# Kernel tuning notes

Measured on AMD Instinct MI355X. Metric: run time of the kernel, lower is better.

## Reference

```python
import jax, jax.numpy as jnp
import numpy as np

B, NSP, H, W = 8, 1024, 256, 256   # frames, superpixels/frame, label-map size
N = B * NSP                        # total superpixel nodes
MIX = 0.5                          # mixing_coeff
SIGMA = 0.05


def _interp_axis(x, out, axis):
    # 1-D bilinear interpolation along `axis`, align_corners=True
    n = x.shape[axis]
    pos = jnp.linspace(0.0, n - 1.0, out).astype(x.dtype)
    i0 = jnp.floor(pos).astype(jnp.int32)
    i1 = jnp.minimum(i0 + 1, n - 1)
    wt = pos - i0.astype(x.dtype)
    shp = [1] * x.ndim
    shp[axis] = out
    wt = wt.reshape(shp)
    return jnp.take(x, i0, axis=axis) * (1 - wt) + jnp.take(x, i1, axis=axis) * wt


def _upsample_ac(x, oh, ow):
    # nn.UpsamplingBilinear2d (align_corners=True)
    if x.shape[2] == oh and x.shape[3] == ow:
        return x
    return _interp_axis(_interp_axis(x, oh, 2), ow, 3)


def _sp_pool(feats, seg):
    # upsample [B,C,h,w] to label resolution, then average features per superpixel -> [N, C]
    C = feats.shape[1]
    up = _upsample_ac(feats, H, W)
    vals = up.transpose(0, 2, 3, 1).reshape(-1, C)          # [B*H*W, C]
    sums = jax.ops.segment_sum(vals, seg, num_segments=N)
    cnt = jax.ops.segment_sum(jnp.ones((seg.shape[0],), vals.dtype), seg, num_segments=N)
    return sums / jnp.maximum(cnt, 1.0)[:, None]


def _gcn(x, Wm, b, src, dst, ew):
    # GCNConv(normalize=False): out_i = sum_{j->i} ew * (x_j @ W) + b
    h = x @ Wm
    agg = jax.ops.segment_sum(h[src] * ew[:, None], dst, num_segments=x.shape[0])
    return agg + b


def _coord_map():
    # channel 0 varies along dim2 (w), channel 1 varies along dim3 (h), both in [0,1]
    c0 = jnp.broadcast_to((jnp.arange(H, dtype=jnp.float32) / (H - 1))[:, None], (H, W))
    c1 = jnp.broadcast_to((jnp.arange(W, dtype=jnp.float32) / (W - 1))[None, :], (H, W))
    return jnp.broadcast_to(jnp.stack([c0, c1], 0)[None], (B, 2, H, W))


def setup_inputs() -> dict:
    key = jax.random.key(0)
    ks = jax.random.split(key, 12)
    labels = jax.random.randint(ks[0], (B, 1, H, W), 0, NSP, dtype=jnp.int32)
    skip0 = jax.random.normal(ks[1], (B, 512, 32, 32), jnp.float32)
    skip1 = jax.random.normal(ks[2], (B, 256, 64, 64), jnp.float32)
    skip2 = jax.random.normal(ks[3], (B, 256, 128, 128), jnp.float32)
    E = 131072
    edges_nn = jax.random.randint(ks[4], (2, E), 0, N, dtype=jnp.int32)
    negs = jax.random.randint(ks[5], (E,), 0, N, dtype=jnp.int32)
    W0 = jax.random.normal(ks[6], (512, 256), jnp.float32) / np.float32(np.sqrt(512))
    W1 = jax.random.normal(ks[7], (256, 256), jnp.float32) / np.float32(np.sqrt(256))
    W2 = jax.random.normal(ks[8], (256, 256), jnp.float32) / np.float32(np.sqrt(256))
    lin_w = jax.random.normal(ks[9], (256, 1), jnp.float32) / np.float32(np.sqrt(256))
    z = jnp.zeros((256,), jnp.float32)
    return {"labels": labels, "skip0": skip0, "skip1": skip1, "skip2": skip2,
            "edges_nn": edges_nn, "negs": negs,
            "W0": W0, "b0": z, "W1": W1, "b1": z, "W2": W2, "b2": z, "lin_w": lin_w}


def reference(labels, skip0, skip1, skip2, edges_nn, negs, W0, b0, W1, b1, W2, b2, lin_w):
    # per-pixel global superpixel id (offset per frame)
    seg = (labels.reshape(B, -1) + NSP * jnp.arange(B, dtype=labels.dtype)[:, None]).reshape(-1)
    src, dst = edges_nn[0], edges_nn[1]

    # pooled normalized coordinates per superpixel -> gaussian edge weights
    pc = _sp_pool(_coord_map(), seg)                        # [N, 2]
    dr = pc[src] - pc[dst]
    dist = jnp.linalg.norm(dr, axis=1)
    edge_attr = jnp.exp(-dist ** 2 / SIGMA)

    x = _sp_pool(skip0, seg)                                # [N, 512]
    layers = [(W0, b0, None), (W1, b1, skip1), (W2, b2, skip2)]
    for i, (Wm, b, sk) in enumerate(layers):
        if i > 0:
            x = (1 - MIX) * x + MIX * _sp_pool(sk, seg)
        x = jax.nn.relu(_gcn(x, Wm, b, src, dst, edge_attr))

    s = x @ lin_w                                           # [N, 1]
    dap = jax.nn.sigmoid(s[src] - s[dst])
    dan = jax.nn.sigmoid(s[src] - s[negs])
    return dan, dap, edge_attr
```

## Files before the change

### kernel.cpp

```cpp
#include <hip/hip_runtime.h>
#include <hip/hip_bf16.h>
#include <cstdint>
#include <cstddef>

#define BB 8
#define NSPX 1024
#define NNODE 8192
#define EE 131072
#define NPIX 524288
#define CH 256

using bf16 = __hip_bfloat16;
typedef unsigned int uint;
typedef unsigned long long u64;

__device__ __forceinline__ float blo(uint u) { return __uint_as_float(u << 16); }
__device__ __forceinline__ float bhi(uint u) { return __uint_as_float(u & 0xffff0000u); }

__global__ __launch_bounds__(256) void zero_kernel(int4* p, int n4) {
  int i = blockIdx.x * 256 + threadIdx.x;
  int stride = gridDim.x * 256;
  int4 z = make_int4(0, 0, 0, 0);
  for (; i < n4; i += stride) p[i] = z;
}

__global__ __launch_bounds__(256) void seg_cnt_kernel(const int* __restrict__ labels,
                                                      int* __restrict__ segb,
                                                      u64* __restrict__ packed) {
  int p = blockIdx.x * 256 + threadIdx.x;
  if (p >= NPIX) return;
  int b = p >> 16;
  int h = (p >> 8) & 255;
  int w = p & 255;
  int seg = labels[p] + (b << 10);
  segb[p] = seg;
  u64 enc = (1ULL << 48) | ((u64)h << 24) | (u64)w;
  atomicAdd(&packed[seg], enc);
}

__global__ __launch_bounds__(256) void rcnt_kernel(const u64* __restrict__ packed,
                                                   int* __restrict__ cnt, float* __restrict__ rcnt,
                                                   float* __restrict__ pch, float* __restrict__ pcw) {
  int n = blockIdx.x * 256 + threadIdx.x;
  if (n >= NNODE) return;
  u64 v = packed[n];
  int c = (int)(v >> 48);
  int sh = (int)((v >> 24) & 0xFFFFFF);
  int sw = (int)(v & 0xFFFFFF);
  cnt[n] = c;
  float r = 1.0f / (float)(c > 1 ? c : 1);
  rcnt[n] = r;
  pch[n] = (float)sh * r * (1.0f / 255.0f);
  pcw[n] = (float)sw * r * (1.0f / 255.0f);
}

__global__ __launch_bounds__(1024) void scan_kernel(const int* __restrict__ cin, int* __restrict__ coff) {
  __shared__ int ps[1024];
  int t = threadIdx.x;
  int base = t * 8;
  int v[8];
  int sum = 0;
#pragma unroll
  for (int i = 0; i < 8; ++i) {
    int x = cin[base + i];
    v[i] = sum;
    sum += x;
  }
  ps[t] = sum;
  __syncthreads();
  for (int off = 1; off < 1024; off <<= 1) {
    int x = (t >= off) ? ps[t - off] : 0;
    __syncthreads();
    ps[t] += x;
    __syncthreads();
  }
  int prev = (t == 0) ? 0 : ps[t - 1];
#pragma unroll
  for (int i = 0; i < 8; ++i) coff[base + i] = prev + v[i];
  if (t == 1023) coff[8192] = ps[1023];
}

__global__ __launch_bounds__(256) void edge_cnt_kernel(const int* __restrict__ dst, int* __restrict__ cnt_e) {
  int e = blockIdx.x * 256 + threadIdx.x;
  if (e < EE) atomicAdd(&cnt_e[dst[e]], 1);
}

__global__ __launch_bounds__(256) void edge_attr_kernel(const int* __restrict__ src, const int* __restrict__ dst,
                                                        const float* __restrict__ pch, const float* __restrict__ pcw,
                                                        float* __restrict__ ew, float* __restrict__ outp) {
  int e = blockIdx.x * 256 + threadIdx.x;
  if (e >= EE) return;
  int s1 = src[e], d1 = dst[e];
  float dh = pch[s1] - pch[d1];
  float dw = pcw[s1] - pcw[d1];
  float ea = expf(-(dh * dh + dw * dw) * 20.0f);
  ew[e] = ea;
  outp[2 * EE + e] = ea;
}

__global__ __launch_bounds__(256) void edge_scatter_kernel(const int* __restrict__ dst,
                                                           const int* __restrict__ src,
                                                           const float* __restrict__ ew,
                                                           const int* __restrict__ eoff,
                                                           int* __restrict__ ecur,
                                                           int* __restrict__ srcs,
                                                           float* __restrict__ ews) {
  int e = blockIdx.x * 256 + threadIdx.x;
  if (e >= EE) return;
  int d = dst[e];
  int pos = eoff[d] + atomicAdd(&ecur[d], 1);
  srcs[pos] = src[e];
  ews[pos] = ew[e];
}

__global__ __launch_bounds__(256) void pixel_scatter_kernel(const int* __restrict__ segb,
                                                            const int* __restrict__ poff,
                                                            int* __restrict__ pcur,
                                                            int* __restrict__ psorted) {
  int p = blockIdx.x * 256 + threadIdx.x;
  if (p >= NPIX) return;
  int s = segb[p];
  int pos = poff[s] + atomicAdd(&pcur[s], 1);
  psorted[pos] = p;
}

__global__ __launch_bounds__(256) void gemm_kmaj_bf16(const float* __restrict__ A,
                                                      const float* __restrict__ W,
                                                      bf16* __restrict__ out) {
  __shared__ float As[64][36];
  int b = blockIdx.z;
  int m0 = blockIdx.x * 32;
  int n0 = blockIdx.y * 128;
  int t = threadIdx.x;
  int ct = t & 31;
  int rm = t >> 5;
  int l8 = t & 7, kr = t >> 3;
  const float* Ab = A + (size_t)b * 512 * 1024;
  float4 acc[4];
#pragma unroll
  for (int i = 0; i < 4; ++i) acc[i] = make_float4(0.f, 0.f, 0.f, 0.f);
  for (int k0 = 0; k0 < 512; k0 += 64) {
#pragma unroll
    for (int pass = 0; pass < 2; ++pass) {
      int k = kr + pass * 32;
      float4 v = *(const float4*)&Ab[(size_t)(k0 + k) * 1024 + m0 + l8 * 4];
      *(float4*)&As[k][l8 * 4] = v;
    }
    __syncthreads();
#pragma unroll 8
    for (int k = 0; k < 64; ++k) {
      float4 a = *(const float4*)&As[k][rm * 4];
      float4 wv = *(const float4*)&W[(size_t)(k0 + k) * 256 + n0 + ct * 4];
      acc[0].x += a.x * wv.x; acc[0].y += a.x * wv.y; acc[0].z += a.x * wv.z; acc[0].w += a.x * wv.w;
      acc[1].x += a.y * wv.x; acc[1].y += a.y * wv.y; acc[1].z += a.y * wv.z; acc[1].w += a.y * wv.w;
      acc[2].x += a.z * wv.x; acc[2].y += a.z * wv.y; acc[2].z += a.z * wv.z; acc[2].w += a.z * wv.w;
      acc[3].x += a.w * wv.x; acc[3].y += a.w * wv.y; acc[3].z += a.w * wv.z; acc[3].w += a.w * wv.w;
    }
    __syncthreads();
  }
#pragma unroll
  for (int i = 0; i < 4; ++i) {
    int m = m0 + rm * 4 + i;
    __hip_bfloat162 lo = __float22bfloat162_rn(make_float2(acc[i].x, acc[i].y));
    __hip_bfloat162 hi = __float22bfloat162_rn(make_float2(acc[i].z, acc[i].w));
    uint2 pk = make_uint2(*reinterpret_cast<uint*>(&lo), *reinterpret_cast<uint*>(&hi));
    *(uint2*)&out[((size_t)b * 1024 + m) * 256 + n0 + ct * 4] = pk;
  }
}

__global__ __launch_bounds__(256) void transpose64_bf16(const float* __restrict__ src, bf16* __restrict__ dst,
                                                        int C, int P) {
  __shared__ float tile[64][65];
  int b = blockIdx.z;
  int p0 = blockIdx.x * 64;
  int c0 = blockIdx.y * 64;
  int t = threadIdx.x;
  int l16 = t & 15, r16 = t >> 4;
#pragma unroll
  for (int pass = 0; pass < 4; ++pass) {
    int c = r16 + pass * 16;
    float4 v = *(const float4*)&src[((size_t)b * C + c0 + c) * P + p0 + l16 * 4];
    tile[c][l16 * 4 + 0] = v.x;
    tile[c][l16 * 4 + 1] = v.y;
    tile[c][l16 * 4 + 2] = v.z;
    tile[c][l16 * 4 + 3] = v.w;
  }
  __syncthreads();
  int l8 = t & 7, r32 = t >> 3;
#pragma unroll
  for (int pass = 0; pass < 2; ++pass) {
    int p = r32 + pass * 32;
    uint r[4];
#pragma unroll
    for (int q = 0; q < 4; ++q) {
      __hip_bfloat162 h2 = __float22bfloat162_rn(make_float2(tile[l8 * 8 + 2 * q][p], tile[l8 * 8 + 2 * q + 1][p]));
      r[q] = *reinterpret_cast<uint*>(&h2);
    }
    *(uint4*)&dst[((size_t)b * P + p0 + p) * C + c0 + l8 * 8] = make_uint4(r[0], r[1], r[2], r[3]);
  }
}

__device__ __forceinline__ void accum8(float wt, uint4 u, float* a) {
  a[0] += wt * blo(u.x); a[1] += wt * bhi(u.x);
  a[2] += wt * blo(u.y); a[3] += wt * bhi(u.y);
  a[4] += wt * blo(u.z); a[5] += wt * bhi(u.z);
  a[6] += wt * blo(u.w); a[7] += wt * bhi(u.w);
}

template <int HS, int LPP>
__global__ __launch_bounds__(256) void gather_scale(const bf16* __restrict__ F,
                                                    const int* __restrict__ poff,
                                                    const int* __restrict__ psorted,
                                                    const float* __restrict__ rc,
                                                    float* __restrict__ pout) {
  constexpr int S = 256 / LPP;
  constexpr int CHUNK = LPP * 8;
  int blk = blockIdx.x;
  int n = ((blk & 7) << 10) | (blk >> 3);
  int b = n >> 10;
  int c0 = blockIdx.y * CHUNK;
  int t = threadIdx.x;
  int l = t & (LPP - 1);
  int s = t / LPP;
  const bf16* fb = F + (size_t)b * (HS * HS) * 256 + c0 + l * 8;
  const float fh = (float)(HS - 1) / 255.0f;
  int j1 = poff[n + 1];
  float acc[8];
#pragma unroll
  for (int i = 0; i < 8; ++i) acc[i] = 0.f;
  for (int j = poff[n] + s; j < j1; j += S) {
    int p = psorted[j];
    int h = (p >> 8) & 255, w = p & 255;
    float ph = h * fh, pw = w * fh;
    int i0 = (int)ph, j0 = (int)pw;
    float th = ph - (float)i0, tw = pw - (float)j0;
    int i1 = min(i0 + 1, HS - 1), jj1 = min(j0 + 1, HS - 1);
    float w11 = th * tw, w10 = th - w11, w01 = tw - w11, w00 = 1.f - th - tw + w11;
    uint4 u00 = *(const uint4*)(fb + (i0 * HS + j0) * 256);
    uint4 u01 = *(const uint4*)(fb + (i0 * HS + jj1) * 256);
    uint4 u10 = *(const uint4*)(fb + (i1 * HS + j0) * 256);
    uint4 u11 = *(const uint4*)(fb + (i1 * HS + jj1) * 256);
    accum8(w00, u00, acc);
    accum8(w01, u01, acc);
    accum8(w10, u10, acc);
    accum8(w11, u11, acc);
  }
  __shared__ float4 red4[512];
  red4[t * 2 + 0] = make_float4(acc[0], acc[1], acc[2], acc[3]);
  red4[t * 2 + 1] = make_float4(acc[4], acc[5], acc[6], acc[7]);
  __syncthreads();
  if (t < LPP * 2) {
    float r = rc[n];
    int l2 = t >> 1, half = t & 1;
    float4 sum = make_float4(0.f, 0.f, 0.f, 0.f);
#pragma unroll
    for (int ss = 0; ss < S; ++ss) {
      float4 v = red4[(ss * LPP + l2) * 2 + half];
      sum.x += v.x; sum.y += v.y; sum.z += v.z; sum.w += v.w;
    }
    sum.x *= r; sum.y *= r; sum.z *= r; sum.w *= r;
    *(float4*)&pout[(size_t)n * 256 + c0 + t * 4] = sum;
  }
}

__global__ __launch_bounds__(256) void gemm_mix_n256(const float* __restrict__ X, const float* __restrict__ Pl,
                                                     const float* __restrict__ W, float* __restrict__ out) {
  const int t = threadIdx.x;
  const int r0 = blockIdx.x * 16;
  const int cw = (t & 63) * 4;
  const int rg = (t >> 6) * 4;
  __shared__ float Xl[16][68];
  float4 acc[4];
#pragma unroll
  for (int i = 0; i < 4; ++i) acc[i] = make_float4(0.f, 0.f, 0.f, 0.f);
  for (int k0 = 0; k0 < 256; k0 += 64) {
#pragma unroll
    for (int l = 0; l < 4; ++l) {
      int idx = t + 256 * l;
      int r = idx >> 6, k = idx & 63;
      size_t a = (size_t)(r0 + r) * 256 + k0 + k;
      Xl[r][k] = 0.5f * (X[a] + Pl[a]);
    }
    __syncthreads();
#pragma unroll
    for (int k4 = 0; k4 < 64; k4 += 4) {
      float4 a[4];
#pragma unroll
      for (int i = 0; i < 4; ++i) a[i] = *(const float4*)&Xl[rg + i][k4];
#pragma unroll
      for (int kk = 0; kk < 4; ++kk) {
        float4 w = *(const float4*)&W[(size_t)(k0 + k4 + kk) * 256 + cw];
#pragma unroll
        for (int i = 0; i < 4; ++i) {
          float av = ((const float*)&a[i])[kk];
          acc[i].x += av * w.x;
          acc[i].y += av * w.y;
          acc[i].z += av * w.z;
          acc[i].w += av * w.w;
        }
      }
    }
    __syncthreads();
  }
#pragma unroll
  for (int i = 0; i < 4; ++i)
    *(float4*)&out[(size_t)(r0 + rg + i) * 256 + cw] = acc[i];
}

__global__ __launch_bounds__(256) void agg_kernel(const float* __restrict__ h, const float* __restrict__ bias,
                                                  const int* __restrict__ eoff,
                                                  const int* __restrict__ srcs, const float* __restrict__ ews,
                                                  float* __restrict__ xout) {
  int n = blockIdx.x;
  int c = threadIdx.x;
  int e0 = eoff[n], e1 = eoff[n + 1];
  float acc = 0.f;
  for (int j = e0; j < e1; ++j) {
    acc += ews[j] * h[((size_t)srcs[j] << 8) + c];
  }
  float v = acc + bias[c];
  xout[((size_t)n << 8) + c] = v > 0.f ? v : 0.f;
}

__global__ __launch_bounds__(256) void score_kernel(const float* __restrict__ x, const float* __restrict__ lw,
                                                    float* __restrict__ s) {
  int t = threadIdx.x;
  int n = blockIdx.x * 4 + (t >> 6);
  int lane = t & 63;
  const float* row = x + ((size_t)n << 8);
  float v = row[lane] * lw[lane] + row[lane + 64] * lw[lane + 64] +
            row[lane + 128] * lw[lane + 128] + row[lane + 192] * lw[lane + 192];
#pragma unroll
  for (int off = 32; off > 0; off >>= 1) v += __shfl_down(v, off, 64);
  if (lane == 0) s[n] = v;
}

__global__ __launch_bounds__(256) void out_kernel(const float* __restrict__ s, const int* __restrict__ src,
                                                  const int* __restrict__ dst, const int* __restrict__ negs,
                                                  float* __restrict__ outp) {
  int e = blockIdx.x * 256 + threadIdx.x;
  if (e >= EE) return;
  float ss = s[src[e]];
  float a = ss - s[negs[e]];
  float b = ss - s[dst[e]];
  outp[e] = 1.0f / (1.0f + expf(-a));
  outp[EE + e] = 1.0f / (1.0f + expf(-b));
}

extern "C" void kernel_launch(void* const* d_in, const int* in_sizes, int n_in,
                              void* d_out, int out_size, void* d_ws, size_t ws_size,
                              hipStream_t stream) {
  const int*   labels = (const int*)d_in[0];
  const float* skip0  = (const float*)d_in[1];
  const float* skip1  = (const float*)d_in[2];
  const float* skip2  = (const float*)d_in[3];
  const int*   edges  = (const int*)d_in[4];
  const int*   negs   = (const int*)d_in[5];
  const float* W0     = (const float*)d_in[6];
  const float* b0     = (const float*)d_in[7];
  const float* W1     = (const float*)d_in[8];
  const float* b1     = (const float*)d_in[9];
  const float* W2     = (const float*)d_in[10];
  const float* b2     = (const float*)d_in[11];
  const float* lw     = (const float*)d_in[12];
  const int* esrc = edges;
  const int* edst = edges + EE;
  float* outp = (float*)d_out;

  size_t o = 0;
  char* base = (char*)d_ws;
  auto alloc = [&](size_t bytes) -> void* {
    void* p = base + o;
    o += (bytes + 255) & ~(size_t)255;
    return p;
  };
  u64* packed  = (u64*)alloc(NNODE * 8);
  int* cnt_e   = (int*)alloc(NNODE * 4);
  int* ecur    = (int*)alloc(NNODE * 4);
  int* pcur    = (int*)alloc(NNODE * 4);
  size_t zbytes = o;
  int*   cntp    = (int*)alloc(NNODE * 4);
  float* rcnt    = (float*)alloc(NNODE * 4);
  float* pch     = (float*)alloc(NNODE * 4);
  float* pcw     = (float*)alloc(NNODE * 4);
  int*   poff    = (int*)alloc((NNODE + 1) * 4);
  int*   eoff    = (int*)alloc((NNODE + 1) * 4);
  int*   srcs    = (int*)alloc(EE * 4);
  float* ews     = (float*)alloc(EE * 4);
  int*   psorted = (int*)alloc(NPIX * 4);
  float* ewb     = (float*)alloc(EE * 4);
  int*   segb    = (int*)alloc(NPIX * 4);
  float* bufA    = (float*)alloc((size_t)NNODE * CH * 4);
  float* bufB    = (float*)alloc((size_t)NNODE * CH * 4);
  float* bufC    = (float*)alloc((size_t)NNODE * CH * 4);
  float* p1buf   = (float*)alloc((size_t)NNODE * CH * 4);
  float* p2buf   = (float*)alloc((size_t)NNODE * CH * 4);
  bf16*  F0b     = (bf16*)alloc((size_t)BB * 1024 * CH * 2);
  bf16*  F1t     = (bf16*)alloc((size_t)BB * 4096 * CH * 2);
  bf16*  F2t     = (bf16*)alloc((size_t)BB * 16384 * CH * 2);
  float* sbuf    = (float*)alloc(NNODE * 4);
  (void)ws_size; (void)n_in; (void)in_sizes; (void)out_size;

  zero_kernel<<<64, 256, 0, stream>>>((int4*)d_ws, (int)(zbytes / 16));
  seg_cnt_kernel<<<NPIX / 256, 256, 0, stream>>>(labels, segb, packed);
  rcnt_kernel<<<NNODE / 256, 256, 0, stream>>>(packed, cntp, rcnt, pch, pcw);
  scan_kernel<<<1, 1024, 0, stream>>>(cntp, poff);
  pixel_scatter_kernel<<<NPIX / 256, 256, 0, stream>>>(segb, poff, pcur, psorted);
  edge_cnt_kernel<<<EE / 256, 256, 0, stream>>>(edst, cnt_e);
  scan_kernel<<<1, 1024, 0, stream>>>(cnt_e, eoff);
  edge_attr_kernel<<<EE / 256, 256, 0, stream>>>(esrc, edst, pch, pcw, ewb, outp);
  edge_scatter_kernel<<<EE / 256, 256, 0, stream>>>(edst, esrc, ewb, eoff, ecur, srcs, ews);
  gemm_kmaj_bf16<<<dim3(32, 2, BB), 256, 0, stream>>>(skip0, W0, F0b);
  transpose64_bf16<<<dim3(4096 / 64, 4, BB), 256, 0, stream>>>(skip1, F1t, 256, 4096);
  transpose64_bf16<<<dim3(16384 / 64, 4, BB), 256, 0, stream>>>(skip2, F2t, 256, 16384);
  gather_scale<32, 32><<<dim3(NNODE, 1), 256, 0, stream>>>(F0b, poff, psorted, rcnt, bufA);
  gather_scale<64, 32><<<dim3(NNODE, 1), 256, 0, stream>>>(F1t, poff, psorted, rcnt, p1buf);
  gather_scale<128, 16><<<dim3(NNODE, 2), 256, 0, stream>>>(F2t, poff, psorted, rcnt, p2buf);
  agg_kernel<<<NNODE, 256, 0, stream>>>(bufA, b0, eoff, srcs, ews, bufB);
  gemm_mix_n256<<<NNODE / 16, 256, 0, stream>>>(bufB, p1buf, W1, bufC);
  agg_kernel<<<NNODE, 256, 0, stream>>>(bufC, b1, eoff, srcs, ews, bufA);
  gemm_mix_n256<<<NNODE / 16, 256, 0, stream>>>(bufA, p2buf, W2, bufC);
  agg_kernel<<<NNODE, 256, 0, stream>>>(bufC, b2, eoff, srcs, ews, bufB);
  score_kernel<<<NNODE / 4, 256, 0, stream>>>(bufB, lw, sbuf);
  out_kernel<<<EE / 256, 256, 0, stream>>>(sbuf, esrc, edst, negs, outp);
}
```

Baseline: 774.7 us.

## Fuse preprocessing kernels, merge skip0/skip1 gathers, store GCN features as bf16

Merges the pixel and edge counting, both prefix scans, and the pixel/edge scatter plus edge-attribute computation into combined launches, cutting the preprocessing launch count. The skip0 and skip1 gathers now share one pass over each superpixel's sorted pixel list. Edge source and weight are packed into one uint2 array. The GCN hidden features fed to aggregation are stored in bf16, with two channels per thread, to halve gather traffic. This trades some precision in the aggregated features for fewer launches and less memory traffic.

```diff
diff --git a/kernel.cpp b/kernel.cpp
--- a/kernel.cpp
+++ b/kernel.cpp
@@ -16,6 +16,10 @@
 
 __device__ __forceinline__ float blo(uint u) { return __uint_as_float(u << 16); }
 __device__ __forceinline__ float bhi(uint u) { return __uint_as_float(u & 0xffff0000u); }
+__device__ __forceinline__ uint packbf2(float a, float b) {
+  __hip_bfloat162 h = __float22bfloat162_rn(make_float2(a, b));
+  return *reinterpret_cast<uint*>(&h);
+}
 
 __global__ __launch_bounds__(256) void zero_kernel(int4* p, int n4) {
   int i = blockIdx.x * 256 + threadIdx.x;
@@ -24,22 +28,60 @@
   for (; i < n4; i += stride) p[i] = z;
 }
 
-__global__ __launch_bounds__(256) void seg_cnt_kernel(const int* __restrict__ labels,
-                                                      int* __restrict__ segb,
-                                                      u64* __restrict__ packed) {
-  int p = blockIdx.x * 256 + threadIdx.x;
-  if (p >= NPIX) return;
-  int b = p >> 16;
-  int h = (p >> 8) & 255;
-  int w = p & 255;
-  int seg = labels[p] + (b << 10);
-  segb[p] = seg;
-  u64 enc = (1ULL << 48) | ((u64)h << 24) | (u64)w;
-  atomicAdd(&packed[seg], enc);
+__global__ __launch_bounds__(256) void cnt2_kernel(const int* __restrict__ labels,
+                                                   const int* __restrict__ edst,
+                                                   int* __restrict__ segb,
+                                                   u64* __restrict__ packed,
+                                                   int* __restrict__ cnt_e) {
+  int blk = blockIdx.x;
+  int t = threadIdx.x;
+  if (blk < 2048) {
+    int p = blk * 256 + t;
+    int b = p >> 16;
+    int h = (p >> 8) & 255;
+    int w = p & 255;
+    int seg = labels[p] + (b << 10);
+    segb[p] = seg;
+    u64 enc = (1ULL << 48) | ((u64)h << 24) | (u64)w;
+    atomicAdd(&packed[seg], enc);
+  } else {
+    int e = (blk - 2048) * 256 + t;
+    atomicAdd(&cnt_e[edst[e]], 1);
+  }
+}
+
+__global__ __launch_bounds__(1024) void scan2_kernel(const u64* __restrict__ packed,
+                                                     const int* __restrict__ cnt_e,
+                                                     int* __restrict__ poff, int* __restrict__ eoff) {
+  __shared__ int ps[1024];
+  int which = blockIdx.x;
+  int* coff = which ? eoff : poff;
+  int t = threadIdx.x;
+  int base = t * 8;
+  int v[8];
+  int sum = 0;
+#pragma unroll
+  for (int i = 0; i < 8; ++i) {
+    int x = which ? cnt_e[base + i] : (int)(packed[base + i] >> 48);
+    v[i] = sum;
+    sum += x;
+  }
+  ps[t] = sum;
+  __syncthreads();
+  for (int off = 1; off < 1024; off <<= 1) {
+    int x = (t >= off) ? ps[t - off] : 0;
+    __syncthreads();
+    ps[t] += x;
+    __syncthreads();
+  }
+  int prev = (t == 0) ? 0 : ps[t - 1];
+#pragma unroll
+  for (int i = 0; i < 8; ++i) coff[base + i] = prev + v[i];
+  if (t == 1023) coff[8192] = ps[1023];
 }
 
 __global__ __launch_bounds__(256) void rcnt_kernel(const u64* __restrict__ packed,
-                                                   int* __restrict__ cnt, float* __restrict__ rcnt,
+                                                   float* __restrict__ rcnt,
                                                    float* __restrict__ pch, float* __restrict__ pcw) {
   int n = blockIdx.x * 256 + threadIdx.x;
   if (n >= NNODE) return;
@@ -47,81 +89,41 @@
   int c = (int)(v >> 48);
   int sh = (int)((v >> 24) & 0xFFFFFF);
   int sw = (int)(v & 0xFFFFFF);
-  cnt[n] = c;
   float r = 1.0f / (float)(c > 1 ? c : 1);
   rcnt[n] = r;
   pch[n] = (float)sh * r * (1.0f / 255.0f);
   pcw[n] = (float)sw * r * (1.0f / 255.0f);
 }
 
-__global__ __launch_bounds__(1024) void scan_kernel(const int* __restrict__ cin, int* __restrict__ coff) {
-  __shared__ int ps[1024];
-  int t = threadIdx.x;
-  int base = t * 8;
-  int v[8];
-  int sum = 0;
-#pragma unroll
-  for (int i = 0; i < 8; ++i) {
-    int x = cin[base + i];
-    v[i] = sum;
-    sum += x;
-  }
-  ps[t] = sum;
-  __syncthreads();
-  for (int off = 1; off < 1024; off <<= 1) {
-    int x = (t >= off) ? ps[t - off] : 0;
-    __syncthreads();
-    ps[t] += x;
-    __syncthreads();
-  }
-  int prev = (t == 0) ? 0 : ps[t - 1];
-#pragma unroll
-  for (int i = 0; i < 8; ++i) coff[base + i] = prev + v[i];
-  if (t == 1023) coff[8192] = ps[1023];
-}
-
-__global__ __launch_bounds__(256) void edge_cnt_kernel(const int* __restrict__ dst, int* __restrict__ cnt_e) {
-  int e = blockIdx.x * 256 + threadIdx.x;
-  if (e < EE) atomicAdd(&cnt_e[dst[e]], 1);
-}
-
-__global__ __launch_bounds__(256) void edge_attr_kernel(const int* __restrict__ src, const int* __restrict__ dst,
-                                                        const float* __restrict__ pch, const float* __restrict__ pcw,
-                                                        float* __restrict__ ew, float* __restrict__ outp) {
-  int e = blockIdx.x * 256 + threadIdx.x;
-  if (e >= EE) return;
-  int s1 = src[e], d1 = dst[e];
-  float dh = pch[s1] - pch[d1];
-  float dw = pcw[s1] - pcw[d1];
-  float ea = expf(-(dh * dh + dw * dw) * 20.0f);
-  ew[e] = ea;
-  outp[2 * EE + e] = ea;
-}
-
-__global__ __launch_bounds__(256) void edge_scatter_kernel(const int* __restrict__ dst,
-                                                           const int* __restrict__ src,
-                                                           const float* __restrict__ ew,
-                                                           const int* __restrict__ eoff,
-                                                           int* __restrict__ ecur,
-                                                           int* __restrict__ srcs,
-                                                           float* __restrict__ ews) {
-  int e = blockIdx.x * 256 + threadIdx.x;
-  if (e >= EE) return;
-  int d = dst[e];
-  int pos = eoff[d] + atomicAdd(&ecur[d], 1);
-  srcs[pos] = src[e];
-  ews[pos] = ew[e];
-}
-
-__global__ __launch_bounds__(256) void pixel_scatter_kernel(const int* __restrict__ segb,
-                                                            const int* __restrict__ poff,
-                                                            int* __restrict__ pcur,
-                                                            int* __restrict__ psorted) {
-  int p = blockIdx.x * 256 + threadIdx.x;
-  if (p >= NPIX) return;
-  int s = segb[p];
-  int pos = poff[s] + atomicAdd(&pcur[s], 1);
-  psorted[pos] = p;
+__global__ __launch_bounds__(256) void scatter2_kernel(const int* __restrict__ segb,
+                                                       const int* __restrict__ poff,
+                                                       int* __restrict__ pcur,
+                                                       int* __restrict__ psorted,
+                                                       const int* __restrict__ esrc,
+                                                       const int* __restrict__ edst,
+                                                       const float* __restrict__ pch,
+                                                       const float* __restrict__ pcw,
+                                                       const int* __restrict__ eoff,
+                                                       int* __restrict__ ecur,
+                                                       uint2* __restrict__ evw,
+                                                       float* __restrict__ outp) {
+  int blk = blockIdx.x;
+  int t = threadIdx.x;
+  if (blk < 2048) {
+    int p = blk * 256 + t;
+    int s = segb[p];
+    int pos = poff[s] + atomicAdd(&pcur[s], 1);
+    psorted[pos] = p;
+  } else {
+    int e = (blk - 2048) * 256 + t;
+    int s1 = esrc[e], d1 = edst[e];
+    float dh = pch[s1] - pch[d1];
+    float dw = pcw[s1] - pcw[d1];
+    float ea = expf(-(dh * dh + dw * dw) * 20.0f);
+    outp[2 * EE + e] = ea;
+    int pos = eoff[d1] + atomicAdd(&ecur[d1], 1);
+    evw[pos] = make_uint2((uint)s1, __float_as_uint(ea));
+  }
 }
 
 __global__ __launch_bounds__(256) void gemm_kmaj_bf16(const float* __restrict__ A,
@@ -161,9 +163,7 @@
 #pragma unroll
   for (int i = 0; i < 4; ++i) {
     int m = m0 + rm * 4 + i;
-    __hip_bfloat162 lo = __float22bfloat162_rn(make_float2(acc[i].x, acc[i].y));
-    __hip_bfloat162 hi = __float22bfloat162_rn(make_float2(acc[i].z, acc[i].w));
-    uint2 pk = make_uint2(*reinterpret_cast<uint*>(&lo), *reinterpret_cast<uint*>(&hi));
+    uint2 pk = make_uint2(packbf2(acc[i].x, acc[i].y), packbf2(acc[i].z, acc[i].w));
     *(uint2*)&out[((size_t)b * 1024 + m) * 256 + n0 + ct * 4] = pk;
   }
 }
@@ -192,10 +192,8 @@
     int p = r32 + pass * 32;
     uint r[4];
 #pragma unroll
-    for (int q = 0; q < 4; ++q) {
-      __hip_bfloat162 h2 = __float22bfloat162_rn(make_float2(tile[l8 * 8 + 2 * q][p], tile[l8 * 8 + 2 * q + 1][p]));
-      r[q] = *reinterpret_cast<uint*>(&h2);
-    }
+    for (int q = 0; q < 4; ++q)
+      r[q] = packbf2(tile[l8 * 8 + 2 * q][p], tile[l8 * 8 + 2 * q + 1][p]);
     *(uint4*)&dst[((size_t)b * P + p0 + p) * C + c0 + l8 * 8] = make_uint4(r[0], r[1], r[2], r[3]);
   }
 }
@@ -207,55 +205,106 @@
   a[6] += wt * blo(u.w); a[7] += wt * bhi(u.w);
 }
 
-template <int HS, int LPP>
-__global__ __launch_bounds__(256) void gather_scale(const bf16* __restrict__ F,
-                                                    const int* __restrict__ poff,
-                                                    const int* __restrict__ psorted,
-                                                    const float* __restrict__ rc,
-                                                    float* __restrict__ pout) {
-  constexpr int S = 256 / LPP;
-  constexpr int CHUNK = LPP * 8;
+template <int HS>
+__device__ __forceinline__ void taps_scale(const bf16* __restrict__ fb, int h, int w, float* acc) {
+  const float fh = (float)(HS - 1) / 255.0f;
+  float ph = h * fh, pw = w * fh;
+  int i0 = (int)ph, j0 = (int)pw;
+  float th = ph - (float)i0, tw = pw - (float)j0;
+  int i1 = min(i0 + 1, HS - 1), jj1 = min(j0 + 1, HS - 1);
+  float w11 = th * tw, w10 = th - w11, w01 = tw - w11, w00 = 1.f - th - tw + w11;
+  uint4 u00 = *(const uint4*)(fb + (i0 * HS + j0) * 256);
+  uint4 u01 = *(const uint4*)(fb + (i0 * HS + jj1) * 256);
+  uint4 u10 = *(const uint4*)(fb + (i1 * HS + j0) * 256);
+  uint4 u11 = *(const uint4*)(fb + (i1 * HS + jj1) * 256);
+  accum8(w00, u00, acc);
+  accum8(w01, u01, acc);
+  accum8(w10, u10, acc);
+  accum8(w11, u11, acc);
+}
+
+__global__ __launch_bounds__(256) void gather01_kernel(const bf16* __restrict__ F0,
+                                                       const bf16* __restrict__ F1,
+                                                       const int* __restrict__ poff,
+                                                       const int* __restrict__ psorted,
+                                                       const float* __restrict__ rc,
+                                                       bf16* __restrict__ p0out,
+                                                       float* __restrict__ p1out) {
   int blk = blockIdx.x;
   int n = ((blk & 7) << 10) | (blk >> 3);
   int b = n >> 10;
-  int c0 = blockIdx.y * CHUNK;
-  int t = threadIdx.x;
-  int l = t & (LPP - 1);
-  int s = t / LPP;
-  const bf16* fb = F + (size_t)b * (HS * HS) * 256 + c0 + l * 8;
-  const float fh = (float)(HS - 1) / 255.0f;
+  int t = threadIdx.x;
+  int l = t & 31;
+  int s = t >> 5;
+  const bf16* f0 = F0 + (size_t)b * 1024 * 256 + l * 8;
+  const bf16* f1 = F1 + (size_t)b * 4096 * 256 + l * 8;
+  int j1 = poff[n + 1];
+  float a0[8], a1[8];
+#pragma unroll
+  for (int i = 0; i < 8; ++i) { a0[i] = 0.f; a1[i] = 0.f; }
+  for (int j = poff[n] + s; j < j1; j += 8) {
+    int p = psorted[j];
+    int h = (p >> 8) & 255, w = p & 255;
+    taps_scale<32>(f0, h, w, a0);
+    taps_scale<64>(f1, h, w, a1);
+  }
+  __shared__ float4 red[2][512];
+  red[0][t * 2 + 0] = make_float4(a0[0], a0[1], a0[2], a0[3]);
+  red[0][t * 2 + 1] = make_float4(a0[4], a0[5], a0[6], a0[7]);
+  red[1][t * 2 + 0] = make_float4(a1[0], a1[1], a1[2], a1[3]);
+  red[1][t * 2 + 1] = make_float4(a1[4], a1[5], a1[6], a1[7]);
+  __syncthreads();
+  if (t < 64) {
+    float r = rc[n];
+    int l2 = t >> 1, half = t & 1;
+    float4 s0 = make_float4(0.f, 0.f, 0.f, 0.f), s1 = s0;
+#pragma unroll
+    for (int ss = 0; ss < 8; ++ss) {
+      float4 v0 = red[0][(ss * 32 + l2) * 2 + half];
+      float4 v1 = red[1][(ss * 32 + l2) * 2 + half];
+      s0.x += v0.x; s0.y += v0.y; s0.z += v0.z; s0.w += v0.w;
+      s1.x += v1.x; s1.y += v1.y; s1.z += v1.z; s1.w += v1.w;
+    }
+    s0.x *= r; s0.y *= r; s0.z *= r; s0.w *= r;
+    s1.x *= r; s1.y *= r; s1.z *= r; s1.w *= r;
+    *(uint2*)&p0out[(size_t)n * 256 + 4 * t] = make_uint2(packbf2(s0.x, s0.y), packbf2(s0.z, s0.w));
+    *(float4*)&p1out[(size_t)n * 256 + 4 * t] = s1;
+  }
+}
+
+__global__ __launch_bounds__(256) void gather2_kernel(const bf16* __restrict__ F,
+                                                      const int* __restrict__ poff,
+                                                      const int* __restrict__ psorted,
+                                                      const float* __restrict__ rc,
+                                                      float* __restrict__ pout) {
+  int blk = blockIdx.x;
+  int n = ((blk & 7) << 10) | (blk >> 3);
+  int b = n >> 10;
+  int c0 = blockIdx.y * 128;
+  int t = threadIdx.x;
+  int l = t & 15;
+  int s = t >> 4;
+  const bf16* fb = F + (size_t)b * 16384 * 256 + c0 + l * 8;
   int j1 = poff[n + 1];
   float acc[8];
 #pragma unroll
   for (int i = 0; i < 8; ++i) acc[i] = 0.f;
-  for (int j = poff[n] + s; j < j1; j += S) {
+  for (int j = poff[n] + s; j < j1; j += 16) {
     int p = psorted[j];
     int h = (p >> 8) & 255, w = p & 255;
-    float ph = h * fh, pw = w * fh;
-    int i0 = (int)ph, j0 = (int)pw;
-    float th = ph - (float)i0, tw = pw - (float)j0;
-    int i1 = min(i0 + 1, HS - 1), jj1 = min(j0 + 1, HS - 1);
-    float w11 = th * tw, w10 = th - w11, w01 = tw - w11, w00 = 1.f - th - tw + w11;
-    uint4 u00 = *(const uint4*)(fb + (i0 * HS + j0) * 256);
-    uint4 u01 = *(const uint4*)(fb + (i0 * HS + jj1) * 256);
-    uint4 u10 = *(const uint4*)(fb + (i1 * HS + j0) * 256);
-    uint4 u11 = *(const uint4*)(fb + (i1 * HS + jj1) * 256);
-    accum8(w00, u00, acc);
-    accum8(w01, u01, acc);
-    accum8(w10, u10, acc);
-    accum8(w11, u11, acc);
+    taps_scale<128>(fb, h, w, acc);
   }
   __shared__ float4 red4[512];
   red4[t * 2 + 0] = make_float4(acc[0], acc[1], acc[2], acc[3]);
   red4[t * 2 + 1] = make_float4(acc[4], acc[5], acc[6], acc[7]);
   __syncthreads();
-  if (t < LPP * 2) {
+  if (t < 32) {
     float r = rc[n];
     int l2 = t >> 1, half = t & 1;
     float4 sum = make_float4(0.f, 0.f, 0.f, 0.f);
 #pragma unroll
-    for (int ss = 0; ss < S; ++ss) {
-      float4 v = red4[(ss * LPP + l2) * 2 + half];
+    for (int ss = 0; ss < 16; ++ss) {
+      float4 v = red4[(ss * 16 + l2) * 2 + half];
       sum.x += v.x; sum.y += v.y; sum.z += v.z; sum.w += v.w;
     }
     sum.x *= r; sum.y *= r; sum.z *= r; sum.w *= r;
@@ -264,7 +313,7 @@
 }
 
 __global__ __launch_bounds__(256) void gemm_mix_n256(const float* __restrict__ X, const float* __restrict__ Pl,
-                                                     const float* __restrict__ W, float* __restrict__ out) {
+                                                     const float* __restrict__ W, bf16* __restrict__ out) {
   const int t = threadIdx.x;
   const int r0 = blockIdx.x * 16;
   const int cw = (t & 63) * 4;
@@ -303,23 +352,31 @@
     __syncthreads();
   }
 #pragma unroll
-  for (int i = 0; i < 4; ++i)
-    *(float4*)&out[(size_t)(r0 + rg + i) * 256 + cw] = acc[i];
-}
-
-__global__ __launch_bounds__(256) void agg_kernel(const float* __restrict__ h, const float* __restrict__ bias,
+  for (int i = 0; i < 4; ++i) {
+    uint2 pk = make_uint2(packbf2(acc[i].x, acc[i].y), packbf2(acc[i].z, acc[i].w));
+    *(uint2*)&out[(size_t)(r0 + rg + i) * 256 + cw] = pk;
+  }
+}
+
+__global__ __launch_bounds__(256) void agg_kernel(const bf16* __restrict__ h, const float* __restrict__ bias,
                                                   const int* __restrict__ eoff,
-                                                  const int* __restrict__ srcs, const float* __restrict__ ews,
+                                                  const uint2* __restrict__ evw,
                                                   float* __restrict__ xout) {
-  int n = blockIdx.x;
-  int c = threadIdx.x;
+  int n = blockIdx.x * 2 + (threadIdx.x >> 7);
+  int c2 = threadIdx.x & 127;
   int e0 = eoff[n], e1 = eoff[n + 1];
-  float acc = 0.f;
+  float a0 = 0.f, a1 = 0.f;
   for (int j = e0; j < e1; ++j) {
-    acc += ews[j] * h[((size_t)srcs[j] << 8) + c];
-  }
-  float v = acc + bias[c];
-  xout[((size_t)n << 8) + c] = v > 0.f ? v : 0.f;
+    uint2 ev = evw[j];
+    float wv = __uint_as_float(ev.y);
+    uint hv = *(const uint*)&h[((size_t)ev.x << 8) + c2 * 2];
+    a0 += wv * blo(hv);
+    a1 += wv * bhi(hv);
+  }
+  float v0 = a0 + bias[2 * c2];
+  float v1 = a1 + bias[2 * c2 + 1];
+  float2 st = make_float2(v0 > 0.f ? v0 : 0.f, v1 > 0.f ? v1 : 0.f);
+  *(float2*)&xout[((size_t)n << 8) + 2 * c2] = st;
 }
 
 __global__ __launch_bounds__(256) void score_kernel(const float* __restrict__ x, const float* __restrict__ lw,
@@ -379,22 +436,20 @@
   int* ecur    = (int*)alloc(NNODE * 4);
   int* pcur    = (int*)alloc(NNODE * 4);
   size_t zbytes = o;
-  int*   cntp    = (int*)alloc(NNODE * 4);
   float* rcnt    = (float*)alloc(NNODE * 4);
   float* pch     = (float*)alloc(NNODE * 4);
   float* pcw     = (float*)alloc(NNODE * 4);
   int*   poff    = (int*)alloc((NNODE + 1) * 4);
   int*   eoff    = (int*)alloc((NNODE + 1) * 4);
-  int*   srcs    = (int*)alloc(EE * 4);
-  float* ews     = (float*)alloc(EE * 4);
+  uint2* evw     = (uint2*)alloc((size_t)EE * 8);
   int*   psorted = (int*)alloc(NPIX * 4);
-  float* ewb     = (float*)alloc(EE * 4);
   int*   segb    = (int*)alloc(NPIX * 4);
   float* bufA    = (float*)alloc((size_t)NNODE * CH * 4);
   float* bufB    = (float*)alloc((size_t)NNODE * CH * 4);
-  float* bufC    = (float*)alloc((size_t)NNODE * CH * 4);
   float* p1buf   = (float*)alloc((size_t)NNODE * CH * 4);
   float* p2buf   = (float*)alloc((size_t)NNODE * CH * 4);
+  bf16*  h0b     = (bf16*)alloc((size_t)NNODE * CH * 2);
+  bf16*  h1b     = (bf16*)alloc((size_t)NNODE * CH * 2);
   bf16*  F0b     = (bf16*)alloc((size_t)BB * 1024 * CH * 2);
   bf16*  F1t     = (bf16*)alloc((size_t)BB * 4096 * CH * 2);
   bf16*  F2t     = (bf16*)alloc((size_t)BB * 16384 * CH * 2);
@@ -402,25 +457,21 @@
   (void)ws_size; (void)n_in; (void)in_sizes; (void)out_size;
 
   zero_kernel<<<64, 256, 0, stream>>>((int4*)d_ws, (int)(zbytes / 16));
-  seg_cnt_kernel<<<NPIX / 256, 256, 0, stream>>>(labels, segb, packed);
-  rcnt_kernel<<<NNODE / 256, 256, 0, stream>>>(packed, cntp, rcnt, pch, pcw);
-  scan_kernel<<<1, 1024, 0, stream>>>(cntp, poff);
-  pixel_scatter_kernel<<<NPIX / 256, 256, 0, stream>>>(segb, poff, pcur, psorted);
-  edge_cnt_kernel<<<EE / 256, 256, 0, stream>>>(edst, cnt_e);
-  scan_kernel<<<1, 1024, 0, stream>>>(cnt_e, eoff);
-  edge_attr_kernel<<<EE / 256, 256, 0, stream>>>(esrc, edst, pch, pcw, ewb, outp);
-  edge_scatter_kernel<<<EE / 256, 256, 0, stream>>>(edst, esrc, ewb, eoff, ecur, srcs, ews);
+  cnt2_kernel<<<2048 + 512, 256, 0, stream>>>(labels, edst, segb, packed, cnt_e);
+  scan2_kernel<<<2, 1024, 0, stream>>>(packed, cnt_e, poff, eoff);
+  rcnt_kernel<<<NNODE / 256, 256, 0, stream>>>(packed, rcnt, pch, pcw);
+  scatter2_kernel<<<2048 + 512, 256, 0, stream>>>(segb, poff, pcur, psorted,
+                                                  esrc, edst, pch, pcw, eoff, ecur, evw, outp);
   gemm_kmaj_bf16<<<dim3(32, 2, BB), 256, 0, stream>>>(skip0, W0, F0b);
   transpose64_bf16<<<dim3(4096 / 64, 4, BB), 256, 0, stream>>>(skip1, F1t, 256, 4096);
   transpose64_bf16<<<dim3(16384 / 64, 4, BB), 256, 0, stream>>>(skip2, F2t, 256, 16384);
-  gather_scale<32, 32><<<dim3(NNODE, 1), 256, 0, stream>>>(F0b, poff, psorted, rcnt, bufA);
-  gather_scale<64, 32><<<dim3(NNODE, 1), 256, 0, stream>>>(F1t, poff, psorted, rcnt, p1buf);
-  gather_scale<128, 16><<<dim3(NNODE, 2), 256, 0, stream>>>(F2t, poff, psorted, rcnt, p2buf);
-  agg_kernel<<<NNODE, 256, 0, stream>>>(bufA, b0, eoff, srcs, ews, bufB);
-  gemm_mix_n256<<<NNODE / 16, 256, 0, stream>>>(bufB, p1buf, W1, bufC);
-  agg_kernel<<<NNODE, 256, 0, stream>>>(bufC, b1, eoff, srcs, ews, bufA);
-  gemm_mix_n256<<<NNODE / 16, 256, 0, stream>>>(bufA, p2buf, W2, bufC);
-  agg_kernel<<<NNODE, 256, 0, stream>>>(bufC, b2, eoff, srcs, ews, bufB);
+  gather01_kernel<<<NNODE, 256, 0, stream>>>(F0b, F1t, poff, psorted, rcnt, h0b, p1buf);
+  gather2_kernel<<<dim3(NNODE, 2), 256, 0, stream>>>(F2t, poff, psorted, rcnt, p2buf);
+  agg_kernel<<<NNODE / 2, 256, 0, stream>>>(h0b, b0, eoff, evw, bufB);
+  gemm_mix_n256<<<NNODE / 16, 256, 0, stream>>>(bufB, p1buf, W1, h1b);
+  agg_kernel<<<NNODE / 2, 256, 0, stream>>>(h1b, b1, eoff, evw, bufA);
+  gemm_mix_n256<<<NNODE / 16, 256, 0, stream>>>(bufA, p2buf, W2, h1b);
+  agg_kernel<<<NNODE / 2, 256, 0, stream>>>(h1b, b2, eoff, evw, bufB);
   score_kernel<<<NNODE / 4, 256, 0, stream>>>(bufB, lw, sbuf);
   out_kernel<<<EE / 256, 256, 0, stream>>>(sbuf, esrc, edst, negs, outp);
 }
```

New measurement: 738.0 us. 4.7% less time.
